# Kernel optimization log

Measured on AMD Instinct MI355X. Metric: run time of the kernel, lower is better.

## Reference

```python
import jax, jax.numpy as jnp
import numpy as np

B, C, S, H, NC = 256, 2000, 50, 64, 3


def setup_inputs() -> dict:
    key = jax.random.key(0)
    ks = jax.random.split(key, 7)
    s = 1.0 / np.sqrt(H)  # PyTorch LSTM init scale
    return {
        "x": jax.random.normal(ks[0], (B, C, S), dtype=jnp.float32),
        "W_ih": jax.random.uniform(ks[1], (4 * H, 1), jnp.float32, -s, s),
        "W_hh": jax.random.uniform(ks[2], (4 * H, H), jnp.float32, -s, s),
        "b_ih": jax.random.uniform(ks[3], (4 * H,), jnp.float32, -s, s),
        "b_hh": jax.random.uniform(ks[4], (4 * H,), jnp.float32, -s, s),
        "W_fc": jax.random.uniform(ks[5], (NC, H), jnp.float32, -s, s),
        "b_fc": jax.random.uniform(ks[6], (NC,), jnp.float32, -s, s),
    }


def _lstm_last_h(x_flat, W_ih, W_hh, b_ih, b_hh):
    # x_flat: [N, S, 1] with N = B*C. PyTorch gate order: i, f, g, o.
    N = x_flat.shape[0]
    b = b_ih + b_hh  # [4H]
    # input_dim == 1, so precompute the input contribution for all steps:
    # [N, S, 1] @ [1, 4H] -> [N, S, 4H], then scan over time axis.
    x_proj = x_flat @ W_ih.T + b  # [N, S, 4H]
    xs = jnp.moveaxis(x_proj, 1, 0)  # [S, N, 4H]

    def step(carry, x_t):
        h, c = carry
        gates = x_t + h @ W_hh.T  # [N, 4H]
        i, f, g, o = jnp.split(gates, 4, axis=-1)
        i = jax.nn.sigmoid(i)
        f = jax.nn.sigmoid(f)
        g = jnp.tanh(g)
        o = jax.nn.sigmoid(o)
        c = f * c + i * g
        h = o * jnp.tanh(c)
        return (h, c), None

    h0 = jnp.zeros((N, x_proj.shape[-1] // 4), x_flat.dtype)
    (h_last, _), _ = jax.lax.scan(step, (h0, h0), xs)
    return h_last  # [N, H]


def reference(x, W_ih, W_hh, b_ih, b_hh, W_fc, b_fc):
    Bsz, Nc, Sl = x.shape
    x_flat = x.reshape(Bsz * Nc, Sl, 1)
    h_last = _lstm_last_h(x_flat, W_ih, W_hh, b_ih, b_hh)  # [B*C, H]
    logits = h_last @ W_fc.T + b_fc  # [B*C, NC]
    return logits.reshape(Bsz, Nc, -1)
```

## Files before the change

### kernel.cpp

```cpp
#include <hip/hip_runtime.h>

typedef _Float16 h8 __attribute__((ext_vector_type(8)));
typedef _Float16 h4 __attribute__((ext_vector_type(4)));
typedef float f4 __attribute__((ext_vector_type(4)));

#define SEQ_LEN 50
#define HID 64
#define HS 72

#if __has_builtin(__builtin_amdgcn_exp2f)
#define EXP2(x) __builtin_amdgcn_exp2f(x)
#else
extern "C" __device__ float __ocml_native_exp2_f32(float);
#define EXP2(x) __ocml_native_exp2_f32(x)
#endif
#define RCP(x) __builtin_amdgcn_rcpf(x)

#if __has_builtin(__builtin_amdgcn_mfma_f32_16x16x16f16)
#define HAVE_MFMA16 1
#else
#define HAVE_MFMA16 0
#endif

#define LOG2E  1.442695041f
#define LOG2E2 2.885390082f

__global__ __launch_bounds__(128, 3)
void lstm_fused(const float* __restrict__ x,
                const float* __restrict__ W_ih,
                const float* __restrict__ W_hh,
                const float* __restrict__ b_ih,
                const float* __restrict__ b_hh,
                const float* __restrict__ W_fc,
                const float* __restrict__ b_fc,
                float* __restrict__ out)
{
    __shared__ _Float16 sH[2][16 * HS];
    __shared__ float    sXT[SEQ_LEN * 16];

    const int tid  = threadIdx.x;
    const int wave = tid >> 6;
    const int lane = tid & 63;
    const int col  = lane & 15;
    const int quad = lane >> 4;
    const int seqBase = blockIdx.x << 4;

    for (int i = tid; i < SEQ_LEN * 16; i += 128) {
        const int s = i & 15;
        const int t = i >> 4;
        sXT[t * 16 + s] = x[(size_t)(seqBase + s) * SEQ_LEN + t];
    }
    for (int i = tid; i < 2 * 16 * HS; i += 128)
        ((_Float16*)sH)[i] = (_Float16)0.0f;

    h8 Aw[8][2];
#if HAVE_MFMA16
    h4 Ax[8];
#else
    h8 Ax[8];
#endif
    #pragma unroll
    for (int gi = 0; gi < 4; ++gi) {
        const float scale = (gi == 2) ? LOG2E2 : LOG2E;
        #pragma unroll
        for (int d = 0; d < 2; ++d) {
            const int tt = gi * 2 + d;
            const int n  = (gi * 4 + 2 * wave + d) * 16 + col;
#if HAVE_MFMA16
            h4 axf = {};
#else
            h8 axf = {};
#endif
            if (quad == 0) {
                axf[0] = (_Float16)(W_ih[n] * scale);
                axf[1] = (_Float16)((b_ih[n] + b_hh[n]) * scale);
            }
            Ax[tt] = axf;
            #pragma unroll
            for (int kf = 0; kf < 2; ++kf) {
                const float* wp = W_hh + n * HID + kf * 32 + quad * 8;
                f4 lo = *(const f4*)wp;
                f4 hi = *(const f4*)(wp + 4);
                h8 b;
                b[0] = (_Float16)(lo[0] * scale); b[1] = (_Float16)(lo[1] * scale);
                b[2] = (_Float16)(lo[2] * scale); b[3] = (_Float16)(lo[3] * scale);
                b[4] = (_Float16)(hi[0] * scale); b[5] = (_Float16)(hi[1] * scale);
                b[6] = (_Float16)(hi[2] * scale); b[7] = (_Float16)(hi[3] * scale);
                Aw[tt][kf] = b;
            }
        }
    }

    const f4 z4 = {0.0f, 0.0f, 0.0f, 0.0f};

    float c[2][4];
    #pragma unroll
    for (int d = 0; d < 2; ++d)
        #pragma unroll
        for (int r = 0; r < 4; ++r) c[d][r] = 0.0f;

    __syncthreads();

    #pragma unroll 2
    for (int t = 0; t < SEQ_LEN; ++t) {
        const _Float16* hb = sH[t & 1];
        _Float16*       hw = sH[(t + 1) & 1];

        const float xt = sXT[t * 16 + col];
#if HAVE_MFMA16
        h4 bx = {};
#else
        h8 bx = {};
#endif
        bx[0] = (_Float16)xt;
        bx[1] = (_Float16)1.0f;

        const h8 Bh0 = *(const h8*)(hb + col * HS + quad * 8);
        const h8 Bh1 = *(const h8*)(hb + col * HS + 32 + quad * 8);

        #pragma unroll
        for (int d = 0; d < 2; ++d) {
            f4 acc[4];
            #pragma unroll
            for (int gi = 0; gi < 4; ++gi) {
                const int tt = gi * 2 + d;
#if HAVE_MFMA16
                f4 a = __builtin_amdgcn_mfma_f32_16x16x16f16(Ax[tt], bx, z4, 0, 0, 0);
#else
                f4 a = __builtin_amdgcn_mfma_f32_16x16x32_f16(Ax[tt], bx, z4, 0, 0, 0);
#endif
                a = __builtin_amdgcn_mfma_f32_16x16x32_f16(Aw[tt][0], Bh0, a, 0, 0, 0);
                a = __builtin_amdgcn_mfma_f32_16x16x32_f16(Aw[tt][1], Bh1, a, 0, 0, 0);
                acc[gi] = a;
            }
            h4 hv;
            #pragma unroll
            for (int rp = 0; rp < 2; ++rp) {
                const int r0 = rp * 2, r1 = r0 + 1;
                float EiA = EXP2(-acc[0][r0]);
                float EfA = EXP2(-acc[1][r0]);
                float EgA = EXP2( acc[2][r0]);
                float EoA = EXP2(-acc[3][r0]);
                float EiB = EXP2(-acc[0][r1]);
                float EfB = EXP2(-acc[1][r1]);
                float EgB = EXP2( acc[2][r1]);
                float EoB = EXP2(-acc[3][r1]);
                float piA = 1.0f + EiA, pfA = 1.0f + EfA;
                float pgA = 1.0f + EgA, poA = 1.0f + EoA;
                float piB = 1.0f + EiB, pfB = 1.0f + EfB;
                float pgB = 1.0f + EgB, poB = 1.0f + EoB;
                float t1A = piA * pgA,  t1B = piB * pgB;
                float DA  = pfA * t1A,  DB  = pfB * t1B;
                float vA  = fmaf(EgA, pfA, -pfA) * LOG2E2;
                float vB  = fmaf(EgB, pfB, -pfB) * LOG2E2;
                float numA = fmaf(c[d][r0], t1A, vA);
                float numB = fmaf(c[d][r1], t1B, vB);
                float R   = RCP(DA * DB);
                float cnA = fminf(numA * (R * DB), 40.0f);
                float cnB = fminf(numB * (R * DA), 40.0f);
                c[d][r0] = cnA;
                c[d][r1] = cnB;
                float EcA = EXP2(cnA), EcB = EXP2(cnB);
                float DhA = fmaf(poA, EcA, poA);
                float DhB = fmaf(poB, EcB, poB);
                float R2  = RCP(DhA * DhB);
                float rhA = R2 * DhB,  rhB = R2 * DhA;
                hv[r0] = (_Float16)fmaf(EcA, rhA, -rhA);
                hv[r1] = (_Float16)fmaf(EcB, rhB, -rhB);
            }
            *(h4*)(hw + col * HS + 32 * wave + 16 * d + quad * 4) = hv;
        }
        __syncthreads();
    }

    if (lane < 24) {
        const int sl = wave * 8 + lane / 3;
        const int nc = lane % 3;
        const _Float16* hp = sH[0] + sl * HS;
        float a = b_fc[nc];
        #pragma unroll
        for (int u = 0; u < HID; ++u)
            a = fmaf((float)hp[u], W_fc[nc * HID + u], a);
        out[(size_t)(seqBase + sl) * 3 + nc] = a;
    }
}

extern "C" void kernel_launch(void* const* d_in, const int* in_sizes, int n_in,
                              void* d_out, int out_size, void* d_ws, size_t ws_size,
                              hipStream_t stream) {
    const float* x    = (const float*)d_in[0];
    const float* W_ih = (const float*)d_in[1];
    const float* W_hh = (const float*)d_in[2];
    const float* b_ih = (const float*)d_in[3];
    const float* b_hh = (const float*)d_in[4];
    const float* W_fc = (const float*)d_in[5];
    const float* b_fc = (const float*)d_in[6];
    float* out = (float*)d_out;

    const int nSeq   = in_sizes[0] / SEQ_LEN;
    const int blocks = nSeq / 16;

    hipLaunchKernelGGL(lstm_fused, dim3(blocks), dim3(128), 0, stream,
                       x, W_ih, W_hh, b_ih, b_hh, W_fc, b_fc, out);
}
```

Baseline: 1.752 ms.

## Process two 16-sequence tiles per block to interleave independent recurrences

Each block now handles 32 sequences as two independent 16-sequence tiles, with doubled shared-memory buffers for h and x, and interleaves their MFMA chains and gate math. The register-resident W_hh fragments are reused across both tiles, and the two independent dependency chains give the scheduler more instruction-level parallelism to hide MFMA and transcendental latency. The per-step barrier is shared by both tiles. In exchange, register pressure rises (launch bounds drop from 3 to 2 blocks per SM) and the grid is halved, which reduces the number of resident waves.

```diff
diff --git a/kernel.cpp b/kernel.cpp
--- a/kernel.cpp
+++ b/kernel.cpp
@@ -17,15 +17,18 @@
 #define RCP(x) __builtin_amdgcn_rcpf(x)
 
 #if __has_builtin(__builtin_amdgcn_mfma_f32_16x16x16f16)
-#define HAVE_MFMA16 1
+typedef h4 axv_t;
+#define XMFMA(A,B,C) __builtin_amdgcn_mfma_f32_16x16x16f16(A, B, C, 0, 0, 0)
 #else
-#define HAVE_MFMA16 0
+typedef h8 axv_t;
+#define XMFMA(A,B,C) __builtin_amdgcn_mfma_f32_16x16x32_f16(A, B, C, 0, 0, 0)
 #endif
+#define WMFMA(A,B,C) __builtin_amdgcn_mfma_f32_16x16x32_f16(A, B, C, 0, 0, 0)
 
 #define LOG2E  1.442695041f
 #define LOG2E2 2.885390082f
 
-__global__ __launch_bounds__(128, 3)
+__global__ __launch_bounds__(128, 2)
 void lstm_fused(const float* __restrict__ x,
                 const float* __restrict__ W_ih,
                 const float* __restrict__ W_hh,
@@ -35,30 +38,29 @@
                 const float* __restrict__ b_fc,
                 float* __restrict__ out)
 {
-    __shared__ _Float16 sH[2][16 * HS];
-    __shared__ float    sXT[SEQ_LEN * 16];
+    __shared__ _Float16 sH[2][2][16 * HS];
+    __shared__ float    sXT[2][SEQ_LEN * 16];
 
     const int tid  = threadIdx.x;
     const int wave = tid >> 6;
     const int lane = tid & 63;
     const int col  = lane & 15;
     const int quad = lane >> 4;
-    const int seqBase = blockIdx.x << 4;
-
-    for (int i = tid; i < SEQ_LEN * 16; i += 128) {
-        const int s = i & 15;
-        const int t = i >> 4;
-        sXT[t * 16 + s] = x[(size_t)(seqBase + s) * SEQ_LEN + t];
-    }
-    for (int i = tid; i < 2 * 16 * HS; i += 128)
+    const int seqBase = blockIdx.x << 5;
+
+    #pragma unroll
+    for (int tb = 0; tb < 2; ++tb) {
+        for (int i = tid; i < SEQ_LEN * 16; i += 128) {
+            const int s = i & 15;
+            const int t = i >> 4;
+            sXT[tb][t * 16 + s] = x[(size_t)(seqBase + tb * 16 + s) * SEQ_LEN + t];
+        }
+    }
+    for (int i = tid; i < 2 * 2 * 16 * HS; i += 128)
         ((_Float16*)sH)[i] = (_Float16)0.0f;
 
     h8 Aw[8][2];
-#if HAVE_MFMA16
-    h4 Ax[8];
-#else
-    h8 Ax[8];
-#endif
+    axv_t Ax[8];
     #pragma unroll
     for (int gi = 0; gi < 4; ++gi) {
         const float scale = (gi == 2) ? LOG2E2 : LOG2E;
@@ -66,11 +68,7 @@
         for (int d = 0; d < 2; ++d) {
             const int tt = gi * 2 + d;
             const int n  = (gi * 4 + 2 * wave + d) * 16 + col;
-#if HAVE_MFMA16
-            h4 axf = {};
-#else
-            h8 axf = {};
-#endif
+            axv_t axf = {};
             if (quad == 0) {
                 axf[0] = (_Float16)(W_ih[n] * scale);
                 axf[1] = (_Float16)((b_ih[n] + b_hh[n]) * scale);
@@ -93,82 +91,83 @@
 
     const f4 z4 = {0.0f, 0.0f, 0.0f, 0.0f};
 
-    float c[2][4];
+    float c[2][2][4];
     #pragma unroll
-    for (int d = 0; d < 2; ++d)
-        #pragma unroll
-        for (int r = 0; r < 4; ++r) c[d][r] = 0.0f;
+    for (int tb = 0; tb < 2; ++tb)
+        #pragma unroll
+        for (int d = 0; d < 2; ++d)
+            #pragma unroll
+            for (int r = 0; r < 4; ++r) c[tb][d][r] = 0.0f;
 
     __syncthreads();
 
-    #pragma unroll 2
     for (int t = 0; t < SEQ_LEN; ++t) {
-        const _Float16* hb = sH[t & 1];
-        _Float16*       hw = sH[(t + 1) & 1];
-
-        const float xt = sXT[t * 16 + col];
-#if HAVE_MFMA16
-        h4 bx = {};
-#else
-        h8 bx = {};
-#endif
-        bx[0] = (_Float16)xt;
-        bx[1] = (_Float16)1.0f;
-
-        const h8 Bh0 = *(const h8*)(hb + col * HS + quad * 8);
-        const h8 Bh1 = *(const h8*)(hb + col * HS + 32 + quad * 8);
+        h8 Bh0[2], Bh1[2];
+        axv_t bx[2];
+        #pragma unroll
+        for (int tb = 0; tb < 2; ++tb) {
+            const _Float16* hb = sH[tb][t & 1];
+            axv_t bxv = {};
+            bxv[0] = (_Float16)sXT[tb][t * 16 + col];
+            bxv[1] = (_Float16)1.0f;
+            bx[tb]  = bxv;
+            Bh0[tb] = *(const h8*)(hb + col * HS + quad * 8);
+            Bh1[tb] = *(const h8*)(hb + col * HS + 32 + quad * 8);
+        }
 
         #pragma unroll
         for (int d = 0; d < 2; ++d) {
-            f4 acc[4];
+            f4 acc[2][4];
             #pragma unroll
             for (int gi = 0; gi < 4; ++gi) {
                 const int tt = gi * 2 + d;
-#if HAVE_MFMA16
-                f4 a = __builtin_amdgcn_mfma_f32_16x16x16f16(Ax[tt], bx, z4, 0, 0, 0);
-#else
-                f4 a = __builtin_amdgcn_mfma_f32_16x16x32_f16(Ax[tt], bx, z4, 0, 0, 0);
-#endif
-                a = __builtin_amdgcn_mfma_f32_16x16x32_f16(Aw[tt][0], Bh0, a, 0, 0, 0);
-                a = __builtin_amdgcn_mfma_f32_16x16x32_f16(Aw[tt][1], Bh1, a, 0, 0, 0);
-                acc[gi] = a;
-            }
-            h4 hv;
-            #pragma unroll
-            for (int rp = 0; rp < 2; ++rp) {
-                const int r0 = rp * 2, r1 = r0 + 1;
-                float EiA = EXP2(-acc[0][r0]);
-                float EfA = EXP2(-acc[1][r0]);
-                float EgA = EXP2( acc[2][r0]);
-                float EoA = EXP2(-acc[3][r0]);
-                float EiB = EXP2(-acc[0][r1]);
-                float EfB = EXP2(-acc[1][r1]);
-                float EgB = EXP2( acc[2][r1]);
-                float EoB = EXP2(-acc[3][r1]);
-                float piA = 1.0f + EiA, pfA = 1.0f + EfA;
-                float pgA = 1.0f + EgA, poA = 1.0f + EoA;
-                float piB = 1.0f + EiB, pfB = 1.0f + EfB;
-                float pgB = 1.0f + EgB, poB = 1.0f + EoB;
-                float t1A = piA * pgA,  t1B = piB * pgB;
-                float DA  = pfA * t1A,  DB  = pfB * t1B;
-                float vA  = fmaf(EgA, pfA, -pfA) * LOG2E2;
-                float vB  = fmaf(EgB, pfB, -pfB) * LOG2E2;
-                float numA = fmaf(c[d][r0], t1A, vA);
-                float numB = fmaf(c[d][r1], t1B, vB);
-                float R   = RCP(DA * DB);
-                float cnA = fminf(numA * (R * DB), 40.0f);
-                float cnB = fminf(numB * (R * DA), 40.0f);
-                c[d][r0] = cnA;
-                c[d][r1] = cnB;
-                float EcA = EXP2(cnA), EcB = EXP2(cnB);
-                float DhA = fmaf(poA, EcA, poA);
-                float DhB = fmaf(poB, EcB, poB);
-                float R2  = RCP(DhA * DhB);
-                float rhA = R2 * DhB,  rhB = R2 * DhA;
-                hv[r0] = (_Float16)fmaf(EcA, rhA, -rhA);
-                hv[r1] = (_Float16)fmaf(EcB, rhB, -rhB);
-            }
-            *(h4*)(hw + col * HS + 32 * wave + 16 * d + quad * 4) = hv;
+                #pragma unroll
+                for (int tb = 0; tb < 2; ++tb) {
+                    f4 a = XMFMA(Ax[tt], bx[tb], z4);
+                    a = WMFMA(Aw[tt][0], Bh0[tb], a);
+                    a = WMFMA(Aw[tt][1], Bh1[tb], a);
+                    acc[tb][gi] = a;
+                }
+            }
+            #pragma unroll
+            for (int tb = 0; tb < 2; ++tb) {
+                h4 hv;
+                #pragma unroll
+                for (int rp = 0; rp < 2; ++rp) {
+                    const int r0 = rp * 2, r1 = r0 + 1;
+                    float EiA = EXP2(-acc[tb][0][r0]);
+                    float EfA = EXP2(-acc[tb][1][r0]);
+                    float EgA = EXP2( acc[tb][2][r0]);
+                    float EoA = EXP2(-acc[tb][3][r0]);
+                    float EiB = EXP2(-acc[tb][0][r1]);
+                    float EfB = EXP2(-acc[tb][1][r1]);
+                    float EgB = EXP2( acc[tb][2][r1]);
+                    float EoB = EXP2(-acc[tb][3][r1]);
+                    float piA = 1.0f + EiA, pfA = 1.0f + EfA;
+                    float pgA = 1.0f + EgA, poA = 1.0f + EoA;
+                    float piB = 1.0f + EiB, pfB = 1.0f + EfB;
+                    float pgB = 1.0f + EgB, poB = 1.0f + EoB;
+                    float t1A = piA * pgA,  t1B = piB * pgB;
+                    float DA  = pfA * t1A,  DB  = pfB * t1B;
+                    float vA  = fmaf(EgA, pfA, -pfA) * LOG2E2;
+                    float vB  = fmaf(EgB, pfB, -pfB) * LOG2E2;
+                    float numA = fmaf(c[tb][d][r0], t1A, vA);
+                    float numB = fmaf(c[tb][d][r1], t1B, vB);
+                    float R   = RCP(DA * DB);
+                    float cnA = fminf(numA * (R * DB), 40.0f);
+                    float cnB = fminf(numB * (R * DA), 40.0f);
+                    c[tb][d][r0] = cnA;
+                    c[tb][d][r1] = cnB;
+                    float EcA = EXP2(cnA), EcB = EXP2(cnB);
+                    float DhA = fmaf(poA, EcA, poA);
+                    float DhB = fmaf(poB, EcB, poB);
+                    float R2  = RCP(DhA * DhB);
+                    float rhA = R2 * DhB,  rhB = R2 * DhA;
+                    hv[r0] = (_Float16)fmaf(EcA, rhA, -rhA);
+                    hv[r1] = (_Float16)fmaf(EcB, rhB, -rhB);
+                }
+                *(h4*)(sH[tb][(t + 1) & 1] + col * HS + 32 * wave + 16 * d + quad * 4) = hv;
+            }
         }
         __syncthreads();
     }
@@ -176,12 +175,15 @@
     if (lane < 24) {
         const int sl = wave * 8 + lane / 3;
         const int nc = lane % 3;
-        const _Float16* hp = sH[0] + sl * HS;
-        float a = b_fc[nc];
-        #pragma unroll
-        for (int u = 0; u < HID; ++u)
-            a = fmaf((float)hp[u], W_fc[nc * HID + u], a);
-        out[(size_t)(seqBase + sl) * 3 + nc] = a;
+        #pragma unroll
+        for (int tb = 0; tb < 2; ++tb) {
+            const _Float16* hp = sH[tb][0] + sl * HS;
+            float a = b_fc[nc];
+            #pragma unroll
+            for (int u = 0; u < HID; ++u)
+                a = fmaf((float)hp[u], W_fc[nc * HID + u], a);
+            out[(size_t)(seqBase + tb * 16 + sl) * 3 + nc] = a;
+        }
     }
 }
 
@@ -198,7 +200,7 @@
     float* out = (float*)d_out;
 
     const int nSeq   = in_sizes[0] / SEQ_LEN;
-    const int blocks = nSeq / 16;
+    const int blocks = nSeq / 32;
 
     hipLaunchKernelGGL(lstm_fused, dim3(blocks), dim3(128), 0, stream,
                        x, W_ih, W_hh, b_ih, b_hh, W_fc, b_fc, out);
```

New measurement: 1.804 ms. 3.0% more time.

## Keep LSTM hidden state in registers, one wave per 16 sequences

Applied to the files above, without the earlier changes.

Each wave now computes all 64 hidden units for its own 16 sequences. The hidden state comes out of the MFMA output layout and is fed straight back as the B operand of 16x16x16 MFMAs. This removes the per-timestep LDS write/read of h and the __syncthreads barrier that two cooperating waves needed before. Blocks grow to 256 threads covering 64 sequences, and LDS is used only for staging x and for the final FC. In exchange each wave holds four times as many weight fragments in registers (roughly 160 VGPRs for weights) and runs a longer serial MFMA chain per step, which may cut occupancy.

```diff
diff --git a/kernel.cpp b/kernel.cpp
--- a/kernel.cpp
+++ b/kernel.cpp
@@ -1,12 +1,11 @@
 #include <hip/hip_runtime.h>
 
-typedef _Float16 h8 __attribute__((ext_vector_type(8)));
 typedef _Float16 h4 __attribute__((ext_vector_type(4)));
 typedef float f4 __attribute__((ext_vector_type(4)));
 
 #define SEQ_LEN 50
 #define HID 64
-#define HS 72
+#define FSTRIDE 68
 
 #if __has_builtin(__builtin_amdgcn_exp2f)
 #define EXP2(x) __builtin_amdgcn_exp2f(x)
@@ -16,16 +15,12 @@
 #endif
 #define RCP(x) __builtin_amdgcn_rcpf(x)
 
-#if __has_builtin(__builtin_amdgcn_mfma_f32_16x16x16f16)
-#define HAVE_MFMA16 1
-#else
-#define HAVE_MFMA16 0
-#endif
+#define MFMA16(A,B,C) __builtin_amdgcn_mfma_f32_16x16x16f16(A, B, C, 0, 0, 0)
 
 #define LOG2E  1.442695041f
 #define LOG2E2 2.885390082f
 
-__global__ __launch_bounds__(128, 3)
+__global__ __launch_bounds__(256, 2)
 void lstm_fused(const float* __restrict__ x,
                 const float* __restrict__ W_ih,
                 const float* __restrict__ W_hh,
@@ -35,102 +30,77 @@
                 const float* __restrict__ b_fc,
                 float* __restrict__ out)
 {
-    __shared__ _Float16 sH[2][16 * HS];
-    __shared__ float    sXT[SEQ_LEN * 16];
+    __shared__ float    sXT[SEQ_LEN * 64];
+    __shared__ _Float16 sF[64 * FSTRIDE];
 
     const int tid  = threadIdx.x;
     const int wave = tid >> 6;
     const int lane = tid & 63;
     const int col  = lane & 15;
     const int quad = lane >> 4;
-    const int seqBase = blockIdx.x << 4;
+    const int seqBase = blockIdx.x << 6;
 
-    for (int i = tid; i < SEQ_LEN * 16; i += 128) {
-        const int s = i & 15;
-        const int t = i >> 4;
-        sXT[t * 16 + s] = x[(size_t)(seqBase + s) * SEQ_LEN + t];
+    for (int i = tid; i < SEQ_LEN * 64; i += 256) {
+        const int s = i / SEQ_LEN;
+        const int t = i - s * SEQ_LEN;
+        sXT[t * 64 + s] = x[(size_t)(seqBase + s) * SEQ_LEN + t];
     }
-    for (int i = tid; i < 2 * 16 * HS; i += 128)
-        ((_Float16*)sH)[i] = (_Float16)0.0f;
 
-    h8 Aw[8][2];
-#if HAVE_MFMA16
-    h4 Ax[8];
-#else
-    h8 Ax[8];
-#endif
+    h4 Aw[4][4][4];
+    h4 Ax[4][4];
     #pragma unroll
     for (int gi = 0; gi < 4; ++gi) {
         const float scale = (gi == 2) ? LOG2E2 : LOG2E;
         #pragma unroll
-        for (int d = 0; d < 2; ++d) {
-            const int tt = gi * 2 + d;
-            const int n  = (gi * 4 + 2 * wave + d) * 16 + col;
-#if HAVE_MFMA16
+        for (int dq = 0; dq < 4; ++dq) {
+            const int n = gi * 64 + dq * 16 + col;
             h4 axf = {};
-#else
-            h8 axf = {};
-#endif
             if (quad == 0) {
                 axf[0] = (_Float16)(W_ih[n] * scale);
                 axf[1] = (_Float16)((b_ih[n] + b_hh[n]) * scale);
             }
-            Ax[tt] = axf;
+            Ax[gi][dq] = axf;
             #pragma unroll
-            for (int kf = 0; kf < 2; ++kf) {
-                const float* wp = W_hh + n * HID + kf * 32 + quad * 8;
-                f4 lo = *(const f4*)wp;
-                f4 hi = *(const f4*)(wp + 4);
-                h8 b;
-                b[0] = (_Float16)(lo[0] * scale); b[1] = (_Float16)(lo[1] * scale);
-                b[2] = (_Float16)(lo[2] * scale); b[3] = (_Float16)(lo[3] * scale);
-                b[4] = (_Float16)(hi[0] * scale); b[5] = (_Float16)(hi[1] * scale);
-                b[6] = (_Float16)(hi[2] * scale); b[7] = (_Float16)(hi[3] * scale);
-                Aw[tt][kf] = b;
+            for (int kc = 0; kc < 4; ++kc) {
+                const float* wp = W_hh + (size_t)n * HID + kc * 16 + quad * 4;
+                f4 w = *(const f4*)wp;
+                h4 a;
+                a[0] = (_Float16)(w[0] * scale);
+                a[1] = (_Float16)(w[1] * scale);
+                a[2] = (_Float16)(w[2] * scale);
+                a[3] = (_Float16)(w[3] * scale);
+                Aw[gi][dq][kc] = a;
             }
         }
     }
 
     const f4 z4 = {0.0f, 0.0f, 0.0f, 0.0f};
 
-    float c[2][4];
+    h4 hB[4] = {};
+    float c[4][4];
     #pragma unroll
-    for (int d = 0; d < 2; ++d)
+    for (int dq = 0; dq < 4; ++dq)
         #pragma unroll
-        for (int r = 0; r < 4; ++r) c[d][r] = 0.0f;
+        for (int r = 0; r < 4; ++r) c[dq][r] = 0.0f;
 
     __syncthreads();
 
-    #pragma unroll 2
     for (int t = 0; t < SEQ_LEN; ++t) {
-        const _Float16* hb = sH[t & 1];
-        _Float16*       hw = sH[(t + 1) & 1];
+        const float xt = sXT[t * 64 + wave * 16 + col];
+        h4 bext = {};
+        bext[0] = (_Float16)xt;
+        bext[1] = (_Float16)1.0f;
 
-        const float xt = sXT[t * 16 + col];
-#if HAVE_MFMA16
-        h4 bx = {};
-#else
-        h8 bx = {};
-#endif
-        bx[0] = (_Float16)xt;
-        bx[1] = (_Float16)1.0f;
-
-        const h8 Bh0 = *(const h8*)(hb + col * HS + quad * 8);
-        const h8 Bh1 = *(const h8*)(hb + col * HS + 32 + quad * 8);
-
+        h4 hN[4];
         #pragma unroll
-        for (int d = 0; d < 2; ++d) {
+        for (int dq = 0; dq < 4; ++dq) {
             f4 acc[4];
             #pragma unroll
             for (int gi = 0; gi < 4; ++gi) {
-                const int tt = gi * 2 + d;
-#if HAVE_MFMA16
-                f4 a = __builtin_amdgcn_mfma_f32_16x16x16f16(Ax[tt], bx, z4, 0, 0, 0);
-#else
-                f4 a = __builtin_amdgcn_mfma_f32_16x16x32_f16(Ax[tt], bx, z4, 0, 0, 0);
-#endif
-                a = __builtin_amdgcn_mfma_f32_16x16x32_f16(Aw[tt][0], Bh0, a, 0, 0, 0);
-                a = __builtin_amdgcn_mfma_f32_16x16x32_f16(Aw[tt][1], Bh1, a, 0, 0, 0);
+                f4 a = MFMA16(Ax[gi][dq], bext, z4);
+                #pragma unroll
+                for (int kc = 0; kc < 4; ++kc)
+                    a = MFMA16(Aw[gi][dq][kc], hB[kc], a);
                 acc[gi] = a;
             }
             h4 hv;
@@ -153,13 +123,13 @@
                 float DA  = pfA * t1A,  DB  = pfB * t1B;
                 float vA  = fmaf(EgA, pfA, -pfA) * LOG2E2;
                 float vB  = fmaf(EgB, pfB, -pfB) * LOG2E2;
-                float numA = fmaf(c[d][r0], t1A, vA);
-                float numB = fmaf(c[d][r1], t1B, vB);
+                float numA = fmaf(c[dq][r0], t1A, vA);
+                float numB = fmaf(c[dq][r1], t1B, vB);
                 float R   = RCP(DA * DB);
                 float cnA = fminf(numA * (R * DB), 40.0f);
                 float cnB = fminf(numB * (R * DA), 40.0f);
-                c[d][r0] = cnA;
-                c[d][r1] = cnB;
+                c[dq][r0] = cnA;
+                c[dq][r1] = cnB;
                 float EcA = EXP2(cnA), EcB = EXP2(cnB);
                 float DhA = fmaf(poA, EcA, poA);
                 float DhB = fmaf(poB, EcB, poB);
@@ -168,20 +138,26 @@
                 hv[r0] = (_Float16)fmaf(EcA, rhA, -rhA);
                 hv[r1] = (_Float16)fmaf(EcB, rhB, -rhB);
             }
-            *(h4*)(hw + col * HS + 32 * wave + 16 * d + quad * 4) = hv;
+            hN[dq] = hv;
         }
-        __syncthreads();
+        #pragma unroll
+        for (int dq = 0; dq < 4; ++dq) hB[dq] = hN[dq];
     }
 
-    if (lane < 24) {
-        const int sl = wave * 8 + lane / 3;
+    #pragma unroll
+    for (int dq = 0; dq < 4; ++dq)
+        *(h4*)(sF + (wave * 16 + col) * FSTRIDE + dq * 16 + quad * 4) = hB[dq];
+    __syncthreads();
+
+    if (lane < 48) {
+        const int sl = lane / 3;
         const int nc = lane % 3;
-        const _Float16* hp = sH[0] + sl * HS;
+        const _Float16* hp = sF + (wave * 16 + sl) * FSTRIDE;
         float a = b_fc[nc];
         #pragma unroll
         for (int u = 0; u < HID; ++u)
             a = fmaf((float)hp[u], W_fc[nc * HID + u], a);
-        out[(size_t)(seqBase + sl) * 3 + nc] = a;
+        out[(size_t)(seqBase + wave * 16 + sl) * 3 + nc] = a;
     }
 }
 
@@ -198,8 +174,8 @@
     float* out = (float*)d_out;
 
     const int nSeq   = in_sizes[0] / SEQ_LEN;
-    const int blocks = nSeq / 16;
+    const int blocks = nSeq / 64;
 
-    hipLaunchKernelGGL(lstm_fused, dim3(blocks), dim3(128), 0, stream,
+    hipLaunchKernelGGL(lstm_fused, dim3(blocks), dim3(256), 0, stream,
                        x, W_ih, W_hh, b_ih, b_hh, W_fc, b_fc, out);
 }
```

New measurement: 2.115 ms. +20.7%, slower.
